# Kernel tuning notes

Hardware: AMD Instinct MI355X
Metric: run time of the kernel (lower is better)

## Reference

```python
import jax, jax.numpy as jnp
import numpy as np

B, T, D, H, E, O, A = 8192, 223, 7, 128, 50, 29, 9
IMPUTE_W, LABEL_W = 0.3, 1.0

def setup_inputs() -> dict:
    key = jax.random.key(0)
    ks = jax.random.split(key, 32)
    u = lambda k, shape, fan: jax.random.uniform(k, shape, jnp.float32, -1.0/np.sqrt(fan), 1.0/np.sqrt(fan))
    return {
        'values':    jax.random.normal(ks[0], (B, T, D), jnp.float32),
        'masks':     (jax.random.uniform(ks[1], (B, T, D)) < 0.8).astype(jnp.float32),
        'deltas':    jax.random.uniform(ks[2], (B, T, D), jnp.float32) * 5.0,
        'probs':     jax.nn.softmax(jax.random.normal(ks[3], (B, O), jnp.float32), axis=1),
        'ancillary': jax.random.normal(ks[4], (B, A), jnp.float32),
        'labels':    jax.random.randint(ks[5], (B,), 0, O, jnp.int32),
        'W_td_h': u(ks[6], (H, D), H),  'b_td_h': u(ks[7], (H,), H),
        'W_td_x': u(ks[8], (D, D), D),  'b_td_x': u(ks[9], (D,), D),
        'W_hist': u(ks[10], (D, H), H), 'b_hist': u(ks[11], (D,), H),
        'W_feat': u(ks[12], (D, D), D), 'b_feat': u(ks[13], (D,), D),
        'W_comb': u(ks[14], (D, 2*D), 2*D), 'b_comb': u(ks[15], (D,), 2*D),
        'W_ih': u(ks[16], (4*H, 2*D), H), 'W_hh': u(ks[17], (4*H, H), H),
        'b_ih': u(ks[18], (4*H,), H),     'b_hh': u(ks[19], (4*H,), H),
        'W_anc': u(ks[20], (E, A), A),    'b_anc': u(ks[21], (E,), A),
        'W_cat': u(ks[22], (H, H + E), H + E), 'b_cat': u(ks[23], (H,), H + E),
        'W_out': u(ks[24], (O, H), H),    'b_out': u(ks[25], (O,), H),
    }

def _rits_forward(values, masks, deltas, probs, ancillary,
                  W_td_h, b_td_h, W_td_x, b_td_x, W_hist, b_hist,
                  W_feat, b_feat, W_comb, b_comb, W_ih, W_hh, b_ih, b_hh,
                  W_anc, b_anc, W_cat, b_cat, W_out, b_out):
    Bn = values.shape[0]
    td_x_diag = jnp.diag(W_td_x)                     # diag=True decay uses only diagonal
    Wf = W_feat * (1.0 - jnp.eye(D, dtype=W_feat.dtype))

    def step(carry, xt):
        h, c, xl = carry
        x, m, d = xt                                  # each [B, D]
        gamma_h = jnp.exp(-jax.nn.relu(d @ W_td_h.T + b_td_h))   # [B, H]
        gamma_x = jnp.exp(-jax.nn.relu(d * td_x_diag + b_td_x))  # [B, D]
        h = h * gamma_h
        x_h = h @ W_hist.T + b_hist
        msum = jnp.sum(m) + 1e-5
        xl = xl + jnp.sum(jnp.abs(x - x_h) * m) / msum
        x_c = m * x + (1.0 - m) * x_h
        z_h = x_c @ Wf.T + b_feat
        xl = xl + jnp.sum(jnp.abs(x - z_h) * m) / msum
        alpha = jnp.concatenate([gamma_x, m], axis=1) @ W_comb.T + b_comb
        c_h = alpha * z_h + (1.0 - alpha) * x_h
        xl = xl + jnp.sum(jnp.abs(x - c_h) * m) / msum
        c_c = m * x + (1.0 - m) * c_h
        inputs = jnp.concatenate([c_c, m], axis=1)    # [B, 2D]
        gates = inputs @ W_ih.T + b_ih + h @ W_hh.T + b_hh  # [B, 4H]
        i, f, g, o = jnp.split(gates, 4, axis=1)
        c = jax.nn.sigmoid(f) * c + jax.nn.sigmoid(i) * jnp.tanh(g)
        h = jax.nn.sigmoid(o) * jnp.tanh(c)
        return (h, c, xl), c_c

    h0 = jnp.zeros((Bn, H), values.dtype)
    c0 = jnp.zeros((Bn, H), values.dtype)
    xs = (jnp.swapaxes(values, 0, 1), jnp.swapaxes(masks, 0, 1), jnp.swapaxes(deltas, 0, 1))
    (h, c, x_loss), imps = jax.lax.scan(step, (h0, c0, jnp.float32(0.0)), xs)
    imputations = jnp.swapaxes(imps, 0, 1)           # [B, T, D]

    x_loss = x_loss * IMPUTE_W
    anc = jax.nn.relu(ancillary @ W_anc.T + b_anc)
    h = jax.nn.relu(jnp.concatenate([h, anc], axis=1) @ W_cat.T + b_cat)
    y_h = jax.nn.softmax(h @ W_out.T + b_out, axis=1)
    y_loss = jnp.sum((y_h - probs) ** 2) / (Bn + 1e-5) * LABEL_W
    return x_loss, y_loss, x_loss + y_loss, y_h, imputations

def reference(values, masks, deltas, probs, ancillary, labels,
              W_td_h, b_td_h, W_td_x, b_td_x, W_hist, b_hist,
              W_feat, b_feat, W_comb, b_comb, W_ih, W_hh, b_ih, b_hh,
              W_anc, b_anc, W_cat, b_cat, W_out, b_out):
    x_loss, y_loss, loss, y_h, imputations = _rits_forward(
        values, masks, deltas, probs, ancillary,
        W_td_h, b_td_h, W_td_x, b_td_x, W_hist, b_hist,
        W_feat, b_feat, W_comb, b_comb, W_ih, W_hh, b_ih, b_hh,
        W_anc, b_anc, W_cat, b_cat, W_out, b_out)
    return (x_loss, y_loss, loss, y_h, imputations, labels)
```

## Files before the change

kernel.cpp:

```cpp
#include <hip/hip_runtime.h>
#include <math.h>

#define B_ 8192
#define T_ 223
#define D_ 7
#define H_ 128
#define E_ 50
#define O_ 29
#define A_ 9
#define TD_ (T_*D_)
#define NB 32
#define NTHR 512
#define MB 8
#define MS_BG 128

#define WS_MINV  0
#define WS_ACC   (WS_MINV + T_)
#define WS_WCATT (WS_ACC + 2)
#define WS_HFIN  (WS_WCATT + 178*H_)

#define OUT_YH  3
#define OUT_IMP (OUT_YH + B_*O_)
#define OUT_LAB (OUT_IMP + B_*T_*D_)

typedef __attribute__((ext_vector_type(8))) short short8;
typedef __attribute__((ext_vector_type(4))) float floatx4;
#define MFMA16(Av,Bv,Cv) __builtin_amdgcn_mfma_f32_16x16x32_bf16((Av),(Bv),(Cv),0,0,0)

__device__ __forceinline__ unsigned short f2bf(float f) {
    unsigned int u = __builtin_bit_cast(unsigned int, f);
    return (unsigned short)((u + 0x7FFFu + ((u >> 16) & 1u)) >> 16);
}
__device__ __forceinline__ float bf2f(unsigned short s) {
    unsigned int u = ((unsigned int)s) << 16;
    return __builtin_bit_cast(float, u);
}
__device__ __forceinline__ float rcp_(float x)  { return __builtin_amdgcn_rcpf(x); }
__device__ __forceinline__ float sigm(float x)  { return rcp_(1.f + __expf(-x)); }
__device__ __forceinline__ float tanh_(float x) { return 1.f - 2.f*rcp_(1.f + __expf(2.f*x)); }

__global__ void rits_prep(const float* __restrict__ W_cat, float* __restrict__ ws)
{
    int idx = blockIdx.x * 256 + threadIdx.x;
    if (idx < H_*178) {
        int j = idx / 178, k = idx - j*178;
        ws[WS_WCATT + k*H_ + j] = W_cat[idx];
    }
    if (idx < T_) ws[WS_MINV + idx] = 0.f;
    if (idx < 2) ws[WS_ACC + idx] = 0.f;
}

__global__ void rits_msum(const float* __restrict__ masks, float* __restrict__ ws)
{
    const int tc = blockIdx.x % 7;
    const int bg = blockIdx.x / 7;
    const int t0 = tc * 32;
    const int nt = (t0 + 32 <= T_) ? 32 : (T_ - t0);
    const int ncol = nt * D_;
    const int tid = threadIdx.x;
    __shared__ float sums[224];
    float s = 0.f;
    if (tid < ncol) {
        const int bpg = B_ / MS_BG;
        const float* p = masks + (size_t)bg * bpg * TD_ + (size_t)t0 * D_ + tid;
        #pragma unroll 4
        for (int b = 0; b < bpg; ++b) s += p[(size_t)b * TD_];
    }
    if (tid < 224) sums[tid] = (tid < ncol) ? s : 0.f;
    __syncthreads();
    if (tid < 32) {
        float r = 0.f;
        #pragma unroll
        for (int q = 0; q < 7; ++q) r += sums[tid*7 + q];
        if (t0 + tid < T_) atomicAdd(&ws[WS_MINV + t0 + tid], r);
    }
}

__global__ __launch_bounds__(NTHR, 2) void rits_main(
    const float* __restrict__ values, const float* __restrict__ masks, const float* __restrict__ deltas,
    const float* __restrict__ W_td_h, const float* __restrict__ b_td_h,
    const float* __restrict__ W_td_x, const float* __restrict__ b_td_x,
    const float* __restrict__ W_hist, const float* __restrict__ b_hist,
    const float* __restrict__ W_feat, const float* __restrict__ b_feat,
    const float* __restrict__ W_comb, const float* __restrict__ b_comb,
    const float* __restrict__ W_ih, const float* __restrict__ W_hh,
    const float* __restrict__ b_ih, const float* __restrict__ b_hh,
    float* __restrict__ ws, float* __restrict__ out)
{
    __shared__ __attribute__((aligned(16))) unsigned short hbuf[NB*168];
    __shared__ __attribute__((aligned(16))) unsigned short bbuf[NB*32];
    __shared__ __attribute__((aligned(16))) unsigned short whis_lds[16*136];
    __shared__ float xm_l[NB*18];
    __shared__ float gx_l[NB*9];
    __shared__ float xh_l[NB*10];
    __shared__ float impbuf[NB*16*7];
    __shared__ float red[8];

    const int tid  = threadIdx.x;
    const int b0   = blockIdx.x * NB;
    const int lane = tid & 63;
    const int w    = tid >> 6;
    const int quad = lane >> 4;
    const int l15  = lane & 15;

    for (int i = tid; i < NB*168; i += NTHR) hbuf[i] = 0;
    for (int i = tid; i < NB*32;  i += NTHR) bbuf[i] = 0;
    for (int i = tid; i < 16*136; i += NTHR) {
        int r = i / 136, c = i - r*136;
        whis_lds[i] = (r < 7 && c < 128) ? f2bf(W_hist[r*H_ + c]) : 0;
    }
    __syncthreads();
    if (tid < NB) {
        bbuf[tid*32 + 7]  = 0x3F80;
        bbuf[tid*32 + 15] = 0x3F80;
    }

    short8 whhf[4][4];
    short8 winf_c[4];
    short8 winf_mb[4];
    short8 wtdf;
    float  bh_r[4];
    {
        union UU { short8 v; unsigned short u[8]; } fr;
        #pragma unroll
        for (int c = 0; c < 4; ++c) {
            const int j = (c*8 + w)*16 + l15;
            #pragma unroll
            for (int s = 0; s < 4; ++s) {
                const float* p = W_hh + j*H_ + s*32 + quad*8;
                #pragma unroll
                for (int e = 0; e < 8; ++e) fr.u[e] = f2bf(p[e]);
                whhf[c][s] = fr.v;
            }
            #pragma unroll
            for (int e = 0; e < 8; ++e) {
                int k = quad*8 + e;
                fr.u[e] = (k < 7) ? f2bf(W_ih[j*14 + k]) : (unsigned short)0;
            }
            winf_c[c] = fr.v;
            #pragma unroll
            for (int e = 0; e < 8; ++e) {
                int k = quad*8 + e;
                float v = (k < 7) ? W_ih[j*14 + 7 + k]
                        : ((k == 7) ? (b_ih[j] + b_hh[j]) : 0.f);
                fr.u[e] = f2bf(v);
            }
            winf_mb[c] = fr.v;
        }
        const int j2 = w*16 + l15;
        #pragma unroll
        for (int e = 0; e < 8; ++e) {
            int k = quad*8 + e;
            float v = (k >= 8 && k < 15) ? W_td_h[j2*D_ + (k - 8)]
                    : ((k == 15) ? b_td_h[j2] : 0.f);
            fr.u[e] = f2bf(v);
        }
        wtdf = fr.v;
        #pragma unroll
        for (int r = 0; r < 4; ++r) {
            int f = quad*4 + r;
            bh_r[r] = (quad < 2 && f < 7) ? b_hist[f] : 0.f;
        }
    }

    const bool ldr = (tid < NB*D_);
    const int  lb  = tid / D_, li = tid - (tid/D_)*D_;
    float wfr[7], wcr[14], bfr = 0.f, bcr = 0.f, tdx_own = 0.f, btdx_own = 0.f;
    if (ldr) {
        #pragma unroll
        for (int k = 0; k < 7; ++k)  wfr[k] = (k == li) ? 0.f : W_feat[li*D_ + k];
        #pragma unroll
        for (int k = 0; k < 14; ++k) wcr[k] = W_comb[li*14 + k];
        bfr = b_feat[li];  bcr = b_comb[li];
        tdx_own = W_td_x[li*D_ + li];  btdx_own = b_td_x[li];
    }

    float c_st[2][4] = {{0,0,0,0},{0,0,0,0}};
    float lacc = 0.f;

    const long gbase = (long)(b0 + lb)*TD_ + li;
    float rx = 0.f, rm = 0.f, rd = 0.f;
    if (ldr) { rx = values[gbase]; rm = masks[gbase]; rd = deltas[gbase]; }

    const float* msums = ws + WS_MINV;

    for (int t = 0; t < T_; ++t) {
        if (ldr) {
            float2 s2 = { rx, rm };
            *(float2*)&xm_l[lb*18 + 2*li] = s2;
            gx_l[lb*9 + li] = __expf(-fmaxf(fmaf(rd, tdx_own, btdx_own), 0.f));
            bbuf[lb*32 + li] = f2bf(rm);
        }
        __syncthreads();
        if (ldr && t + 1 < T_) {
            const long g = gbase + (long)(t+1)*D_;
            rx = values[g]; rm = masks[g]; rd = deltas[g];
            bbuf[lb*32 + 8 + li] = f2bf(rd);
        }

        floatx4 acc[4][2];
        #pragma unroll
        for (int c = 0; c < 4; ++c)
            #pragma unroll
            for (int nt = 0; nt < 2; ++nt) { floatx4 z = {0,0,0,0}; acc[c][nt] = z; }
        floatx4 xh0 = {0,0,0,0}, xh1 = {0,0,0,0};
        #pragma unroll
        for (int s = 0; s < 4; ++s) {
            short8 hb0 = *(const short8*)&hbuf[l15*168       + s*32 + quad*8];
            short8 hb1 = *(const short8*)&hbuf[(16+l15)*168  + s*32 + quad*8];
            #pragma unroll
            for (int c = 0; c < 4; ++c) {
                acc[c][0] = MFMA16(whhf[c][s], hb0, acc[c][0]);
                acc[c][1] = MFMA16(whhf[c][s], hb1, acc[c][1]);
            }
            if (w == 7) {
                short8 wh = *(const short8*)&whis_lds[l15*136 + s*32 + quad*8];
                xh0 = MFMA16(wh, hb0, xh0);
                xh1 = MFMA16(wh, hb1, xh1);
            }
        }
        if (w == 7 && quad < 2) {
            #pragma unroll
            for (int nt = 0; nt < 2; ++nt) {
                const int b = nt*16 + l15;
                floatx4 xv = nt ? xh1 : xh0;
                float2 p0 = { xv[0] + bh_r[0], xv[1] + bh_r[1] };
                float2 p1 = { xv[2] + bh_r[2], xv[3] + bh_r[3] };
                *(float2*)&xh_l[b*10 + quad*4]     = p0;
                *(float2*)&xh_l[b*10 + quad*4 + 2] = p1;
            }
        }
        __syncthreads();

        const bool dec = (t + 1 < T_);
        floatx4 g0 = {0,0,0,0}, g1 = {0,0,0,0};
        {
            short8 bb0 = *(const short8*)&bbuf[l15*32      + quad*8];
            short8 bb1 = *(const short8*)&bbuf[(16+l15)*32 + quad*8];
            #pragma unroll
            for (int c = 0; c < 4; ++c) {
                acc[c][0] = MFMA16(winf_mb[c], bb0, acc[c][0]);
                acc[c][1] = MFMA16(winf_mb[c], bb1, acc[c][1]);
            }
            if (dec) {
                floatx4 z = {0,0,0,0};
                g0 = MFMA16(wtdf, bb0, z);
                g1 = MFMA16(wtdf, bb1, z);
            }
        }

        if (ldr) {
            const int b = lb, i = li;
            const float invt = rcp_(msums[t] + 1e-5f);
            const float x = xm_l[b*18 + 2*i], m = xm_l[b*18 + 2*i + 1];
            const float xhv = xh_l[b*10 + i];
            float zh = bfr, al = bcr;
            #pragma unroll
            for (int k = 0; k < 7; ++k) {
                const float xk  = xm_l[b*18 + 2*k];
                const float mk  = xm_l[b*18 + 2*k + 1];
                const float xhk = xh_l[b*10 + k];
                const float xck = mk*xk + (1.f - mk)*xhk;
                zh = fmaf(wfr[k], xck, zh);
                al = fmaf(wcr[k], gx_l[b*9 + k], al);
                al = fmaf(wcr[7+k], mk, al);
            }
            const float ch = al*zh + (1.f - al)*xhv;
            const float cc = m*x + (1.f - m)*ch;
            impbuf[(b*16 + (t & 15))*7 + i] = cc;
            hbuf[b*168 + 128 + i] = f2bf(cc);
            lacc = fmaf((fabsf(x-xhv) + fabsf(x-zh) + fabsf(x-ch)) * m, invt, lacc);
        }
        __syncthreads();

        {
            short8 ib0 = *(const short8*)&hbuf[l15*168      + 128 + quad*8];
            short8 ib1 = *(const short8*)&hbuf[(16+l15)*168 + 128 + quad*8];
            #pragma unroll
            for (int c = 0; c < 4; ++c) {
                acc[c][0] = MFMA16(winf_c[c], ib0, acc[c][0]);
                acc[c][1] = MFMA16(winf_c[c], ib1, acc[c][1]);
            }
        }
        #pragma unroll
        for (int nt = 0; nt < 2; ++nt) {
            const int b = nt*16 + l15;
            floatx4 gg = nt ? g1 : g0;
            float hnv[4];
            #pragma unroll
            for (int r = 0; r < 4; ++r) {
                float ig = acc[0][nt][r], fg = acc[1][nt][r];
                float gv = acc[2][nt][r], og = acc[3][nt][r];
                float cn = sigm(fg)*c_st[nt][r] + sigm(ig)*tanh_(gv);
                c_st[nt][r] = cn;
                float hn = sigm(og)*tanh_(cn);
                if (dec) hn *= __expf(-fmaxf(gg[r], 0.f));
                hnv[r] = hn;
            }
            uint2 pk;
            pk.x = (unsigned)f2bf(hnv[0]) | ((unsigned)f2bf(hnv[1]) << 16);
            pk.y = (unsigned)f2bf(hnv[2]) | ((unsigned)f2bf(hnv[3]) << 16);
            *(uint2*)&hbuf[b*168 + w*16 + quad*4] = pk;
        }

        if ((t & 15) == 15 || t == T_ - 1) {
            const int t0 = t & ~15;
            const int b  = tid >> 4, c16 = tid & 15;
            if (t0 + c16 <= t) {
                float* gp = out + (size_t)OUT_IMP + (size_t)(b0+b)*TD_ + (size_t)(t0+c16)*D_;
                const float* lp = &impbuf[(b*16 + c16)*7];
                #pragma unroll
                for (int e = 0; e < 7; ++e) gp[e] = lp[e];
            }
        }
    }
    __syncthreads();

    for (int off = 32; off > 0; off >>= 1) lacc += __shfl_down(lacc, off, 64);
    if ((tid & 63) == 0) red[tid >> 6] = lacc;
    __syncthreads();
    if (tid == 0) {
        float s = 0.f;
        #pragma unroll
        for (int q = 0; q < 8; ++q) s += red[q];
        atomicAdd(&ws[WS_ACC], s);
    }
    for (int i = tid; i < NB*H_; i += NTHR) {
        int b = i >> 7, j = i & 127;
        ws[WS_HFIN + (size_t)(b0+b)*H_ + j] = bf2f(hbuf[b*168 + j]);
    }
}

__global__ __launch_bounds__(128) void rits_head(
    const float* __restrict__ probs, const float* __restrict__ ancillary, const int* __restrict__ labels,
    const float* __restrict__ W_anc, const float* __restrict__ b_anc,
    const float* __restrict__ b_cat,
    const float* __restrict__ W_out, const float* __restrict__ b_out,
    float* __restrict__ ws, float* __restrict__ out)
{
    __shared__ float hb[MB*H_];
    __shared__ float ancl[MB*52];
    __shared__ float hc[MB*H_];
    __shared__ float lg[MB*32];
    __shared__ float smx[MB], sinv[MB], ysum[MB];
    __shared__ float sq[MB*32];
    const int tid = threadIdx.x;
    const int bb0 = blockIdx.x * MB;

    for (int i = tid; i < MB*H_; i += 128) hb[i] = ws[WS_HFIN + (size_t)bb0*H_ + i];
    for (int i = tid; i < MB*E_; i += 128) {
        int b = i / E_, e = i - b*E_;
        float s = b_anc[e];
        #pragma unroll
        for (int a = 0; a < A_; ++a) s = fmaf(ancillary[(bb0+b)*A_ + a], W_anc[e*A_ + a], s);
        ancl[b*52+e] = fmaxf(s, 0.f);
    }
    __syncthreads();
    {
        const int j = tid;
        float s[MB];
        #pragma unroll
        for (int b = 0; b < MB; ++b) s[b] = b_cat[j];
        const float* wc = ws + WS_WCATT;
        for (int k = 0; k < H_; ++k) {
            float wv = wc[k*H_ + j];
            #pragma unroll
            for (int b = 0; b < MB; ++b) s[b] = fmaf(hb[b*H_+k], wv, s[b]);
        }
        for (int k = 0; k < E_; ++k) {
            float wv = wc[(H_+k)*H_ + j];
            #pragma unroll
            for (int b = 0; b < MB; ++b) s[b] = fmaf(ancl[b*52+k], wv, s[b]);
        }
        #pragma unroll
        for (int b = 0; b < MB; ++b) hc[b*H_+j] = fmaxf(s[b], 0.f);
    }
    __syncthreads();
    for (int i = tid; i < MB*O_; i += 128) {
        int b = i / O_, o = i - b*O_;
        float s = b_out[o];
        for (int k = 0; k < H_; ++k) s = fmaf(hc[b*H_+k], W_out[o*H_+k], s);
        lg[b*32+o] = s;
    }
    __syncthreads();
    if (tid < MB) {
        float mx = -1e30f;
        for (int o = 0; o < O_; ++o) mx = fmaxf(mx, lg[tid*32+o]);
        float se = 0.f;
        for (int o = 0; o < O_; ++o) se += __expf(lg[tid*32+o] - mx);
        smx[tid] = mx; sinv[tid] = 1.f / se;
    }
    __syncthreads();
    for (int i = tid; i < MB*O_; i += 128) {
        int b = i / O_, o = i - b*O_;
        float y = __expf(lg[b*32+o] - smx[b]) * sinv[b];
        out[OUT_YH + (size_t)(bb0+b)*O_ + o] = y;
        float d = y - probs[(size_t)(bb0+b)*O_ + o];
        sq[b*32+o] = d*d;
    }
    __syncthreads();
    if (tid < MB) {
        float s = 0.f;
        for (int o = 0; o < O_; ++o) s += sq[tid*32+o];
        ysum[tid] = s;
        out[OUT_LAB + bb0 + tid] = (float)labels[bb0 + tid];
    }
    __syncthreads();
    if (tid == 0) {
        float s = 0.f;
        #pragma unroll
        for (int b = 0; b < MB; ++b) s += ysum[b];
        atomicAdd(&ws[WS_ACC+1], s);
    }
}

__global__ void rits_fin(const float* __restrict__ ws, float* __restrict__ out)
{
    if (blockIdx.x == 0 && threadIdx.x == 0) {
        float xl = ws[WS_ACC] * 0.3f;
        float yl = ws[WS_ACC+1] * (1.0f / (8192.0f + 1e-5f));
        out[0] = xl; out[1] = yl; out[2] = xl + yl;
    }
}

extern "C" void kernel_launch(void* const* d_in, const int* in_sizes, int n_in,
                              void* d_out, int out_size, void* d_ws, size_t ws_size,
                              hipStream_t stream)
{
    const float* values = (const float*)d_in[0];
    const float* masks  = (const float*)d_in[1];
    const float* deltas = (const float*)d_in[2];
    const float* probs  = (const float*)d_in[3];
    const float* ancil  = (const float*)d_in[4];
    const int*   labels = (const int*)  d_in[5];
    const float* W_td_h = (const float*)d_in[6];
    const float* b_td_h = (const float*)d_in[7];
    const float* W_td_x = (const float*)d_in[8];
    const float* b_td_x = (const float*)d_in[9];
    const float* W_hist = (const float*)d_in[10];
    const float* b_hist = (const float*)d_in[11];
    const float* W_feat = (const float*)d_in[12];
    const float* b_feat = (const float*)d_in[13];
    const float* W_comb = (const float*)d_in[14];
    const float* b_comb = (const float*)d_in[15];
    const float* W_ih   = (const float*)d_in[16];
    const float* W_hh   = (const float*)d_in[17];
    const float* b_ih   = (const float*)d_in[18];
    const float* b_hh   = (const float*)d_in[19];
    const float* W_anc  = (const float*)d_in[20];
    const float* b_anc  = (const float*)d_in[21];
    const float* W_cat  = (const float*)d_in[22];
    const float* b_cat  = (const float*)d_in[23];
    const float* W_out  = (const float*)d_in[24];
    const float* b_out  = (const float*)d_in[25];
    float* ws  = (float*)d_ws;
    float* out = (float*)d_out;

    hipLaunchKernelGGL(rits_prep, dim3((H_*178 + 255)/256), dim3(256), 0, stream, W_cat, ws);
    hipLaunchKernelGGL(rits_msum, dim3(7*MS_BG), dim3(256), 0, stream, masks, ws);
    hipLaunchKernelGGL(rits_main, dim3(B_/NB), dim3(NTHR), 0, stream,
                       values, masks, deltas, W_td_h, b_td_h, W_td_x, b_td_x,
                       W_hist, b_hist, W_feat, b_feat, W_comb, b_comb,
                       W_ih, W_hh, b_ih, b_hh, ws, out);
    hipLaunchKernelGGL(rits_head, dim3(B_/MB), dim3(128), 0, stream,
                       probs, ancil, labels, W_anc, b_anc, b_cat, W_out, b_out, ws, out);
    hipLaunchKernelGGL(rits_fin, dim3(1), dim3(1), 0, stream, ws, out);
}
```

Before: 925.6 us.

## Distribute history regression across waves and remove a per-step barrier

The x_h = W_hist·h projection, previously done by wave 7 alone at the start of each step, now runs as partial MFMAs in every wave right after h is written. Its partial sums go to LDS and are reduced by the next step's imputation threads, which removes one of the three block barriers per timestep. Imputation work is spread as 28 lanes per wave, with cross-lane exchange through ds_bpermute. Gate weights are pre-scaled by log2(e) so activations use raw v_exp_f32, and barriers use s_barrier with only an lgkmcnt wait. The changes add extra MFMAs and LDS partial storage, and they depend on a subtle ordering that relies on the remaining barriers.

```diff
diff --git a/kernel.cpp b/kernel.cpp
--- a/kernel.cpp
+++ b/kernel.cpp
@@ -13,6 +13,7 @@
 #define NTHR 512
 #define MB 8
 #define MS_BG 128
+#define IMPST 115
 
 #define WS_MINV  0
 #define WS_ACC   (WS_MINV + T_)
@@ -27,6 +28,9 @@
 typedef __attribute__((ext_vector_type(4))) float floatx4;
 #define MFMA16(Av,Bv,Cv) __builtin_amdgcn_mfma_f32_16x16x32_bf16((Av),(Bv),(Cv),0,0,0)
 
+#define BARRIER() do { asm volatile("s_waitcnt lgkmcnt(0)" ::: "memory"); \
+                       __builtin_amdgcn_s_barrier(); } while (0)
+
 __device__ __forceinline__ unsigned short f2bf(float f) {
     unsigned int u = __builtin_bit_cast(unsigned int, f);
     return (unsigned short)((u + 0x7FFFu + ((u >> 16) & 1u)) >> 16);
@@ -36,8 +40,11 @@
     return __builtin_bit_cast(float, u);
 }
 __device__ __forceinline__ float rcp_(float x)  { return __builtin_amdgcn_rcpf(x); }
-__device__ __forceinline__ float sigm(float x)  { return rcp_(1.f + __expf(-x)); }
-__device__ __forceinline__ float tanh_(float x) { return 1.f - 2.f*rcp_(1.f + __expf(2.f*x)); }
+__device__ __forceinline__ float exp2_(float x) { float r; asm("v_exp_f32 %0, %1"  : "=v"(r) : "v"(x)); return r; }
+__device__ __forceinline__ float expn2_(float x){ float r; asm("v_exp_f32 %0, -%1" : "=v"(r) : "v"(x)); return r; }
+
+#define L2E   1.44269504088896f
+#define TL2E  2.88539008177793f
 
 __global__ void rits_prep(const float* __restrict__ W_cat, float* __restrict__ ws)
 {
@@ -89,11 +96,11 @@
 {
     __shared__ __attribute__((aligned(16))) unsigned short hbuf[NB*168];
     __shared__ __attribute__((aligned(16))) unsigned short bbuf[NB*32];
-    __shared__ __attribute__((aligned(16))) unsigned short whis_lds[16*136];
+    __shared__ __attribute__((aligned(16))) unsigned short zpad[8];
+    __shared__ float xh_part[8*NB*8];
     __shared__ float xm_l[NB*18];
     __shared__ float gx_l[NB*9];
-    __shared__ float xh_l[NB*10];
-    __shared__ float impbuf[NB*16*7];
+    __shared__ float impbuf[NB*IMPST];
     __shared__ float red[8];
 
     const int tid  = threadIdx.x;
@@ -105,10 +112,8 @@
 
     for (int i = tid; i < NB*168; i += NTHR) hbuf[i] = 0;
     for (int i = tid; i < NB*32;  i += NTHR) bbuf[i] = 0;
-    for (int i = tid; i < 16*136; i += NTHR) {
-        int r = i / 136, c = i - r*136;
-        whis_lds[i] = (r < 7 && c < 128) ? f2bf(W_hist[r*H_ + c]) : 0;
-    }
+    for (int i = tid; i < 8*NB*8; i += NTHR) xh_part[i] = 0.f;
+    if (tid < 8) zpad[tid] = 0;
     __syncthreads();
     if (tid < NB) {
         bbuf[tid*32 + 7]  = 0x3F80;
@@ -119,23 +124,25 @@
     short8 winf_c[4];
     short8 winf_mb[4];
     short8 wtdf;
-    float  bh_r[4];
+    short8 wxf;
     {
+        const float scg[4] = { L2E, L2E, TL2E, L2E };
         union UU { short8 v; unsigned short u[8]; } fr;
         #pragma unroll
         for (int c = 0; c < 4; ++c) {
+            const float sc = scg[c];
             const int j = (c*8 + w)*16 + l15;
             #pragma unroll
             for (int s = 0; s < 4; ++s) {
                 const float* p = W_hh + j*H_ + s*32 + quad*8;
                 #pragma unroll
-                for (int e = 0; e < 8; ++e) fr.u[e] = f2bf(p[e]);
+                for (int e = 0; e < 8; ++e) fr.u[e] = f2bf(p[e] * sc);
                 whhf[c][s] = fr.v;
             }
             #pragma unroll
             for (int e = 0; e < 8; ++e) {
                 int k = quad*8 + e;
-                fr.u[e] = (k < 7) ? f2bf(W_ih[j*14 + k]) : (unsigned short)0;
+                fr.u[e] = (k < 7) ? f2bf(W_ih[j*14 + k] * sc) : (unsigned short)0;
             }
             winf_c[c] = fr.v;
             #pragma unroll
@@ -143,7 +150,7 @@
                 int k = quad*8 + e;
                 float v = (k < 7) ? W_ih[j*14 + 7 + k]
                         : ((k == 7) ? (b_ih[j] + b_hh[j]) : 0.f);
-                fr.u[e] = f2bf(v);
+                fr.u[e] = f2bf(v * sc);
             }
             winf_mb[c] = fr.v;
         }
@@ -153,49 +160,57 @@
             int k = quad*8 + e;
             float v = (k >= 8 && k < 15) ? W_td_h[j2*D_ + (k - 8)]
                     : ((k == 15) ? b_td_h[j2] : 0.f);
-            fr.u[e] = f2bf(v);
+            fr.u[e] = f2bf(v * L2E);
         }
         wtdf = fr.v;
         #pragma unroll
-        for (int r = 0; r < 4; ++r) {
-            int f = quad*4 + r;
-            bh_r[r] = (quad < 2 && f < 7) ? b_hist[f] : 0.f;
-        }
-    }
-
-    const bool ldr = (tid < NB*D_);
-    const int  lb  = tid / D_, li = tid - (tid/D_)*D_;
-    float wfr[7], wcr[14], bfr = 0.f, bcr = 0.f, tdx_own = 0.f, btdx_own = 0.f;
-    if (ldr) {
-        #pragma unroll
-        for (int k = 0; k < 7; ++k)  wfr[k] = (k == li) ? 0.f : W_feat[li*D_ + k];
-        #pragma unroll
-        for (int k = 0; k < 14; ++k) wcr[k] = W_comb[li*14 + k];
-        bfr = b_feat[li];  bcr = b_comb[li];
-        tdx_own = W_td_x[li*D_ + li];  btdx_own = b_td_x[li];
+        for (int e = 0; e < 8; ++e) {
+            int k = quad*8 + e;
+            fr.u[e] = (l15 < 7 && k < 16) ? f2bf(W_hist[l15*H_ + w*16 + k])
+                                          : (unsigned short)0;
+        }
+        wxf = fr.v;
+    }
+
+    const int l7q = lane / 7, l7r = lane - l7q*7;
+    const bool athr = (lane < 28);
+    const int arow = w*4 + l7q;
+    const int afeat = l7r;
+    float wfr[7], wcr[14], bfr = 0.f, bcr = 0.f;
+    float tdx_own = 0.f, btdx_own = 0.f, bh_own = 0.f;
+    if (athr) {
+        #pragma unroll
+        for (int k = 0; k < 7; ++k)  wfr[k] = (k == afeat) ? 0.f : W_feat[afeat*D_ + k];
+        #pragma unroll
+        for (int k = 0; k < 14; ++k) wcr[k] = W_comb[afeat*14 + k];
+        bfr = b_feat[afeat];  bcr = b_comb[afeat];
+        tdx_own = W_td_x[afeat*D_ + afeat] * L2E;
+        btdx_own = b_td_x[afeat] * L2E;
+        bh_own = b_hist[afeat];
     }
 
     float c_st[2][4] = {{0,0,0,0},{0,0,0,0}};
     float lacc = 0.f;
 
-    const long gbase = (long)(b0 + lb)*TD_ + li;
+    const long gbase = (long)(b0 + arow)*TD_ + afeat;
     float rx = 0.f, rm = 0.f, rd = 0.f;
-    if (ldr) { rx = values[gbase]; rm = masks[gbase]; rd = deltas[gbase]; }
+    if (athr) { rx = values[gbase]; rm = masks[gbase]; rd = deltas[gbase]; }
 
     const float* msums = ws + WS_MINV;
 
     for (int t = 0; t < T_; ++t) {
-        if (ldr) {
+        float x_cur = rx, m_cur = rm;
+        if (athr) {
             float2 s2 = { rx, rm };
-            *(float2*)&xm_l[lb*18 + 2*li] = s2;
-            gx_l[lb*9 + li] = __expf(-fmaxf(fmaf(rd, tdx_own, btdx_own), 0.f));
-            bbuf[lb*32 + li] = f2bf(rm);
-        }
-        __syncthreads();
-        if (ldr && t + 1 < T_) {
+            *(float2*)&xm_l[arow*18 + 2*afeat] = s2;
+            gx_l[arow*9 + afeat] = expn2_(fmaxf(fmaf(rd, tdx_own, btdx_own), 0.f));
+            bbuf[arow*32 + afeat] = f2bf(rm);
+        }
+        BARRIER();
+        if (athr && t + 1 < T_) {
             const long g = gbase + (long)(t+1)*D_;
             rx = values[g]; rm = masks[g]; rd = deltas[g];
-            bbuf[lb*32 + 8 + li] = f2bf(rd);
+            bbuf[arow*32 + 8 + afeat] = f2bf(rd);
         }
 
         floatx4 acc[4][2];
@@ -203,7 +218,6 @@
         for (int c = 0; c < 4; ++c)
             #pragma unroll
             for (int nt = 0; nt < 2; ++nt) { floatx4 z = {0,0,0,0}; acc[c][nt] = z; }
-        floatx4 xh0 = {0,0,0,0}, xh1 = {0,0,0,0};
         #pragma unroll
         for (int s = 0; s < 4; ++s) {
             short8 hb0 = *(const short8*)&hbuf[l15*168       + s*32 + quad*8];
@@ -213,27 +227,7 @@
                 acc[c][0] = MFMA16(whhf[c][s], hb0, acc[c][0]);
                 acc[c][1] = MFMA16(whhf[c][s], hb1, acc[c][1]);
             }
-            if (w == 7) {
-                short8 wh = *(const short8*)&whis_lds[l15*136 + s*32 + quad*8];
-                xh0 = MFMA16(wh, hb0, xh0);
-                xh1 = MFMA16(wh, hb1, xh1);
-            }
-        }
-        if (w == 7 && quad < 2) {
-            #pragma unroll
-            for (int nt = 0; nt < 2; ++nt) {
-                const int b = nt*16 + l15;
-                floatx4 xv = nt ? xh1 : xh0;
-                float2 p0 = { xv[0] + bh_r[0], xv[1] + bh_r[1] };
-                float2 p1 = { xv[2] + bh_r[2], xv[3] + bh_r[3] };
-                *(float2*)&xh_l[b*10 + quad*4]     = p0;
-                *(float2*)&xh_l[b*10 + quad*4 + 2] = p1;
-            }
-        }
-        __syncthreads();
-
-        const bool dec = (t + 1 < T_);
-        floatx4 g0 = {0,0,0,0}, g1 = {0,0,0,0};
+        }
         {
             short8 bb0 = *(const short8*)&bbuf[l15*32      + quad*8];
             short8 bb1 = *(const short8*)&bbuf[(16+l15)*32 + quad*8];
@@ -242,36 +236,34 @@
                 acc[c][0] = MFMA16(winf_mb[c], bb0, acc[c][0]);
                 acc[c][1] = MFMA16(winf_mb[c], bb1, acc[c][1]);
             }
-            if (dec) {
-                floatx4 z = {0,0,0,0};
-                g0 = MFMA16(wtdf, bb0, z);
-                g1 = MFMA16(wtdf, bb1, z);
-            }
-        }
-
-        if (ldr) {
-            const int b = lb, i = li;
+        }
+
+        if (athr) {
+            float xh8 = bh_own;
+            #pragma unroll
+            for (int q = 0; q < 8; ++q) xh8 += xh_part[q*(NB*8) + arow*8 + afeat];
             const float invt = rcp_(msums[t] + 1e-5f);
-            const float x = xm_l[b*18 + 2*i], m = xm_l[b*18 + 2*i + 1];
-            const float xhv = xh_l[b*10 + i];
+            const int bl4 = l7q * 7;
             float zh = bfr, al = bcr;
             #pragma unroll
             for (int k = 0; k < 7; ++k) {
-                const float xk  = xm_l[b*18 + 2*k];
-                const float mk  = xm_l[b*18 + 2*k + 1];
-                const float xhk = xh_l[b*10 + k];
-                const float xck = mk*xk + (1.f - mk)*xhk;
+                float xhk = __builtin_bit_cast(float,
+                    __builtin_amdgcn_ds_bpermute((bl4 + k) << 2,
+                        __builtin_bit_cast(int, xh8)));
+                float2 xm2 = *(const float2*)&xm_l[arow*18 + 2*k];
+                float xck = xm2.y*xm2.x + (1.f - xm2.y)*xhk;
                 zh = fmaf(wfr[k], xck, zh);
-                al = fmaf(wcr[k], gx_l[b*9 + k], al);
-                al = fmaf(wcr[7+k], mk, al);
-            }
-            const float ch = al*zh + (1.f - al)*xhv;
-            const float cc = m*x + (1.f - m)*ch;
-            impbuf[(b*16 + (t & 15))*7 + i] = cc;
-            hbuf[b*168 + 128 + i] = f2bf(cc);
-            lacc = fmaf((fabsf(x-xhv) + fabsf(x-zh) + fabsf(x-ch)) * m, invt, lacc);
-        }
-        __syncthreads();
+                al = fmaf(wcr[k], gx_l[arow*9 + k], al);
+                al = fmaf(wcr[7+k], xm2.y, al);
+            }
+            const float ch = al*zh + (1.f - al)*xh8;
+            const float cc = m_cur*x_cur + (1.f - m_cur)*ch;
+            impbuf[arow*IMPST + (t & 15)*7 + afeat] = cc;
+            hbuf[arow*168 + 128 + afeat] = f2bf(cc);
+            lacc = fmaf((fabsf(x_cur-xh8) + fabsf(x_cur-zh) + fabsf(x_cur-ch)) * m_cur,
+                        invt, lacc);
+        }
+        BARRIER();
 
         {
             short8 ib0 = *(const short8*)&hbuf[l15*168      + 128 + quad*8];
@@ -281,6 +273,15 @@
                 acc[c][0] = MFMA16(winf_c[c], ib0, acc[c][0]);
                 acc[c][1] = MFMA16(winf_c[c], ib1, acc[c][1]);
             }
+        }
+        const bool dec = (t + 1 < T_);
+        floatx4 g0 = {0,0,0,0}, g1 = {0,0,0,0};
+        if (dec) {
+            short8 bb0 = *(const short8*)&bbuf[l15*32      + quad*8];
+            short8 bb1 = *(const short8*)&bbuf[(16+l15)*32 + quad*8];
+            floatx4 z = {0,0,0,0};
+            g0 = MFMA16(wtdf, bb0, z);
+            g1 = MFMA16(wtdf, bb1, z);
         }
         #pragma unroll
         for (int nt = 0; nt < 2; ++nt) {
@@ -291,16 +292,37 @@
             for (int r = 0; r < 4; ++r) {
                 float ig = acc[0][nt][r], fg = acc[1][nt][r];
                 float gv = acc[2][nt][r], og = acc[3][nt][r];
-                float cn = sigm(fg)*c_st[nt][r] + sigm(ig)*tanh_(gv);
+                float si = rcp_(1.f + expn2_(ig));
+                float sf = rcp_(1.f + expn2_(fg));
+                float tg = 1.f - 2.f*rcp_(1.f + exp2_(gv));
+                float cn = sf*c_st[nt][r] + si*tg;
                 c_st[nt][r] = cn;
-                float hn = sigm(og)*tanh_(cn);
-                if (dec) hn *= __expf(-fmaxf(gg[r], 0.f));
+                float so = rcp_(1.f + expn2_(og));
+                float th = 1.f - 2.f*rcp_(1.f + exp2_(cn*TL2E));
+                float hn = so*th;
+                if (dec) hn *= expn2_(fmaxf(gg[r], 0.f));
                 hnv[r] = hn;
             }
             uint2 pk;
             pk.x = (unsigned)f2bf(hnv[0]) | ((unsigned)f2bf(hnv[1]) << 16);
             pk.y = (unsigned)f2bf(hnv[2]) | ((unsigned)f2bf(hnv[3]) << 16);
             *(uint2*)&hbuf[b*168 + w*16 + quad*4] = pk;
+        }
+        if (dec) {
+            const unsigned short* a0 = (quad < 2)
+                ? &hbuf[l15*168      + w*16 + quad*8] : zpad;
+            const unsigned short* a1 = (quad < 2)
+                ? &hbuf[(16+l15)*168 + w*16 + quad*8] : zpad;
+            short8 hb0 = *(const short8*)a0;
+            short8 hb1 = *(const short8*)a1;
+            floatx4 z = {0,0,0,0};
+            floatx4 p0 = MFMA16(wxf, hb0, z);
+            floatx4 p1 = MFMA16(wxf, hb1, z);
+            if (quad < 2) {
+                floatx4 q0 = p0, q1 = p1;
+                *(floatx4*)&xh_part[w*(NB*8) + l15*8      + quad*4] = q0;
+                *(floatx4*)&xh_part[w*(NB*8) + (16+l15)*8 + quad*4] = q1;
+            }
         }
 
         if ((t & 15) == 15 || t == T_ - 1) {
@@ -308,13 +330,13 @@
             const int b  = tid >> 4, c16 = tid & 15;
             if (t0 + c16 <= t) {
                 float* gp = out + (size_t)OUT_IMP + (size_t)(b0+b)*TD_ + (size_t)(t0+c16)*D_;
-                const float* lp = &impbuf[(b*16 + c16)*7];
+                const float* lp = &impbuf[b*IMPST + c16*7];
                 #pragma unroll
                 for (int e = 0; e < 7; ++e) gp[e] = lp[e];
             }
         }
     }
-    __syncthreads();
+    BARRIER();
 
     for (int off = 32; off > 0; off >>= 1) lacc += __shfl_down(lacc, off, 64);
     if ((tid & 63) == 0) red[tid >> 6] = lacc;
```

Result: slower. 972.4 us (+5.1%).
